# Kernel tuning notes

Hardware: AMD Instinct MI355X
Metric: run time of the kernel (lower is better)

The kernel has to match this reference:

```python
import jax, jax.numpy as jnp
import numpy as np

STATE_DIM, ACTION_DIM, HIDDEN_DIM = 512, 64, 2048
INPUT_DIM = STATE_DIM + ACTION_DIM + 1  # 577
BATCH = 4096


def setup_inputs() -> dict:
    key = jax.random.key(0)
    ks = jax.random.split(key, 12)
    sc_x = 1.0 / np.sqrt(INPUT_DIM)
    sc_h = 1.0 / np.sqrt(HIDDEN_DIM)
    return {
        "s": jax.random.normal(ks[0], (BATCH, STATE_DIM), jnp.float32),
        "a_prev": jax.random.normal(ks[1], (BATCH, ACTION_DIM), jnp.float32),
        "r_prev": jax.random.normal(ks[2], (BATCH, 1), jnp.float32),
        "h": jnp.zeros((HIDDEN_DIM,), jnp.float32),
        "c": jnp.zeros((HIDDEN_DIM,), jnp.float32),
        # Fused gate weights: columns ordered [i, f, g(c-tilde), o]
        "Wx": jax.random.uniform(ks[3], (INPUT_DIM, 4 * HIDDEN_DIM), jnp.float32, -sc_x, sc_x),
        "Wh": jax.random.uniform(ks[4], (HIDDEN_DIM, 4 * HIDDEN_DIM), jnp.float32, -sc_h, sc_h),
        "bh": jax.random.uniform(ks[5], (4 * HIDDEN_DIM,), jnp.float32, -sc_h, sc_h),
        "Wa": jax.random.uniform(ks[6], (HIDDEN_DIM, ACTION_DIM), jnp.float32, -sc_h, sc_h),
        "ba": jax.random.uniform(ks[7], (ACTION_DIM,), jnp.float32, -sc_h, sc_h),
        "Wv": jax.random.uniform(ks[8], (HIDDEN_DIM, 1), jnp.float32, -sc_h, sc_h),
        "bv": jax.random.uniform(ks[9], (1,), jnp.float32, -sc_h, sc_h),
    }


def reference(s, a_prev, r_prev, h, c, Wx, Wh, bh, Wa, ba, Wv, bv):
    # x: [B, input_dim]
    x = jnp.concatenate([s, a_prev, r_prev], axis=1)
    # Two fused GEMMs replace the 8 separate small linears (same math).
    z = x @ Wx + h @ Wh + bh          # [B, 4H]
    zi, zf, zg, zo = jnp.split(z, 4, axis=-1)
    i = jax.nn.sigmoid(zi)
    f = jax.nn.sigmoid(zf)
    c_new = f * c + i * jnp.tanh(zg)  # [B, H] (c broadcast over batch)
    o = jax.nn.sigmoid(zo)
    h_new = o * jnp.tanh(c_new)       # [B, H]
    probs = jax.nn.softmax(h_new @ Wa + ba, axis=1)  # [B, A]
    v = h_new @ Wv + bv               # [B, 1]
    return (probs, v)
```

## Files before the change

kernel.cpp:

```cpp
#include <hip/hip_runtime.h>
#include <hip/hip_bf16.h>

#define BATCH   4096
#define SDIM    512
#define ADIM    64
#define IDIM    577
#define KP2     640
#define NKT2    10
#define HDIM    2048
#define ZDIM    8192
#define BUFE    (128 * 64)

typedef __attribute__((ext_vector_type(8))) __bf16 bf16x8;
typedef __attribute__((ext_vector_type(4))) float  accx4;

__global__ __launch_bounds__(256) void setup_kernel(
    const float* __restrict__ s, const float* __restrict__ a_prev,
    const float* __restrict__ r_prev, const float* __restrict__ h,
    const float* __restrict__ wx, const float* __restrict__ wh,
    const float* __restrict__ wa,
    __hip_bfloat16* __restrict__ xb, __hip_bfloat16* __restrict__ wxt,
    __hip_bfloat16* __restrict__ waT, float* __restrict__ zh_w)
{
    __shared__ float stile[64 * 33];
    const int bid = blockIdx.x;
    const int t = threadIdx.x;

    if (bid < 2560) {
        const int kt2 = bid >> 8;
        const int nt  = bid & 255;
        const int c  = t & 31, r0 = t >> 5;
#pragma unroll
        for (int i = 0; i < 8; ++i) {
            int r = r0 + i * 8;
            int k = kt2 * 64 + r;
            stile[r * 33 + c] =
                (k < IDIM) ? wx[(size_t)k * ZDIM + nt * 32 + c] : 0.0f;
        }
        __syncthreads();
        const int nr = t >> 3, ch = t & 7;
        bf16x8 w8;
#pragma unroll
        for (int j = 0; j < 8; ++j)
            w8[j] = (__bf16)stile[(ch * 8 + j) * 33 + nr];
        *(bf16x8*)(wxt + (size_t)(nt * 32 + nr) * KP2 + kt2 * 64 + ch * 8) = w8;
    } else if (bid < 2816) {
        const int zb = bid - 2560;
        const int nb = zb & 31, ky = zb >> 5;
        const int n  = nb * 256 + t;
        const float* hp  = h + ky * 256;
        const float* whp = wh + (size_t)ky * 256 * ZDIM + n;
        float p = 0.0f;
#pragma unroll 16
        for (int kk = 0; kk < 256; ++kk)
            p = fmaf(hp[kk], whp[(size_t)kk * ZDIM], p);
        zh_w[ky * ZDIM + n] = p;
    } else if (bid < 6912) {
        const int row = bid - 2816;
        const float* srow = s + (size_t)row * SDIM;
        const float* arow = a_prev + (size_t)row * ADIM;
        __hip_bfloat16* xrow = xb + (size_t)row * KP2;
        for (int c = t; c < KP2; c += 256) {
            float v;
            if (c < SDIM)        v = srow[c];
            else if (c < 576)    v = arow[c - SDIM];
            else if (c == 576)   v = r_prev[row];
            else                 v = 0.0f;
            xrow[c] = __float2bfloat16(v);
        }
    } else {
        const int wb = bid - 6912;
        const int kt = wb >> 1, at = wb & 1;
        const int c  = t & 31, r0 = t >> 5;
#pragma unroll
        for (int i = 0; i < 4; ++i) {
            int r = r0 + i * 8;
            stile[r * 33 + c] = wa[(size_t)(kt * 32 + r) * ADIM + at * 32 + c];
        }
        __syncthreads();
#pragma unroll
        for (int i = 0; i < 4; ++i) {
            int r = r0 + i * 8;
            waT[(size_t)(at * 32 + r) * HDIM + kt * 32 + c] =
                __float2bfloat16(stile[c * 33 + r]);
        }
    }
}

__device__ __forceinline__ float sigmoid_f(float x) {
    return 1.0f / (1.0f + __expf(-x));
}
__device__ __forceinline__ float tanh_f(float x) {
    return 1.0f - 2.0f / (1.0f + __expf(2.0f * x));
}

__global__ __launch_bounds__(256, 2) void lstm_gemm(
    const __hip_bfloat16* __restrict__ xb,
    const __hip_bfloat16* __restrict__ wxt,
    const float* __restrict__ zh_w,
    const float* __restrict__ bh,
    const float* __restrict__ cvec,
    __hip_bfloat16* __restrict__ hout)
{
    __shared__ __bf16 smA[2 * BUFE];
    __shared__ __bf16 smB[2 * BUFE];
    const int t    = threadIdx.x;
    const int lane = t & 63;
    const int wid  = t >> 6;
    const int m0   = blockIdx.x * 128;
    const int n0   = blockIdx.y * 32;
    const int wm   = wid >> 1, wn = wid & 1;
    const int fl15 = lane & 15;
    const int fhi  = lane >> 4;

    accx4 acc[4][4] = {};

    const int srow = lane >> 3;
    const int slot = lane & 7;
    const int cch  = slot ^ srow;
    const __bf16* gA[4]; const __bf16* gB[4];
    __bf16* lA[4]; __bf16* lB[4];
#pragma unroll
    for (int i = 0; i < 4; ++i) {
        const int r = wid * 32 + i * 8 + srow;
        gA[i] = (const __bf16*)xb + (size_t)(m0 + r) * KP2 + cch * 8;
        const int g = r >> 5, nn = r & 31;
        gB[i] = (const __bf16*)wxt +
                (size_t)(g * HDIM + n0 + nn) * KP2 + cch * 8;
        lA[i] = smA + (wid * 32 + i * 8) * 64;
        lB[i] = smB + (wid * 32 + i * 8) * 64;
    }

    auto stage = [&](int tile, int p) {
        const int ko = tile * 64;
        const int po = p * BUFE;
#pragma unroll
        for (int i = 0; i < 4; ++i) {
            __builtin_amdgcn_global_load_lds(
                (const __attribute__((address_space(1))) void*)(gA[i] + ko),
                (__attribute__((address_space(3))) void*)(lA[i] + po),
                16, 0, 0);
            __builtin_amdgcn_global_load_lds(
                (const __attribute__((address_space(1))) void*)(gB[i] + ko),
                (__attribute__((address_space(3))) void*)(lB[i] + po),
                16, 0, 0);
        }
    };

    auto compute = [&](int p) {
        const int po = p * BUFE;
#pragma unroll
        for (int hf = 0; hf < 2; ++hf) {
            const int sl = ((hf * 4 + fhi) ^ slot) * 8;
            bf16x8 af[4], bfr[4];
#pragma unroll
            for (int rt = 0; rt < 4; ++rt)
                af[rt] = *(const bf16x8*)(smA + po +
                    (wm * 64 + rt * 16 + fl15) * 64 + sl);
#pragma unroll
            for (int g = 0; g < 4; ++g)
                bfr[g] = *(const bf16x8*)(smB + po +
                    (g * 32 + wn * 16 + fl15) * 64 + sl);
#pragma unroll
            for (int g = 0; g < 4; ++g)
#pragma unroll
                for (int rt = 0; rt < 4; ++rt)
                    acc[g][rt] = __builtin_amdgcn_mfma_f32_16x16x32_bf16(
                        af[rt], bfr[g], acc[g][rt], 0, 0, 0);
        }
    };

    stage(0, 0);
    __syncthreads();
#pragma unroll
    for (int kt = 0; kt < NKT2 - 1; ++kt) {
        stage(kt + 1, (kt + 1) & 1);
        compute(kt & 1);
        __syncthreads();
    }
    compute((NKT2 - 1) & 1);

    const int colg = n0 + wn * 16 + fl15;
    float zsum[4];
#pragma unroll
    for (int g = 0; g < 4; ++g) {
        float z = bh[g * HDIM + colg];
#pragma unroll
        for (int j = 0; j < 8; ++j)
            z += zh_w[j * ZDIM + g * HDIM + colg];
        zsum[g] = z;
    }
    const float cv = cvec[colg];
#pragma unroll
    for (int rt = 0; rt < 4; ++rt) {
#pragma unroll
        for (int r = 0; r < 4; ++r) {
            const int row = m0 + wm * 64 + rt * 16 + (fhi << 2) + r;
            const float zi = acc[0][rt][r] + zsum[0];
            const float zf = acc[1][rt][r] + zsum[1];
            const float zg = acc[2][rt][r] + zsum[2];
            const float zo = acc[3][rt][r] + zsum[3];
            const float cn = sigmoid_f(zf) * cv + sigmoid_f(zi) * tanh_f(zg);
            const float hn = sigmoid_f(zo) * tanh_f(cn);
            hout[(size_t)row * HDIM + colg] = __float2bfloat16(hn);
        }
    }
}

__global__ __launch_bounds__(512) void head_kernel(
    const __hip_bfloat16* __restrict__ hnew,
    const __hip_bfloat16* __restrict__ waT,
    const float* __restrict__ wv,
    const float* __restrict__ ba, const float* __restrict__ bv,
    float* __restrict__ probs, float* __restrict__ vout)
{
    __shared__ float lg[2][16][68];
    __shared__ float vpart[2][16];
    const int t    = threadIdx.x;
    const int lane = t & 63;
    const int wid  = t >> 6;
    const int kh   = wid >> 2;
    const int wid2 = wid & 3;
    const int r0   = blockIdx.x * 16;
    const int fl15 = lane & 15, fhi = lane >> 4;

    const __bf16* arow = (const __bf16*)hnew +
        (size_t)(r0 + fl15) * HDIM + kh * 1024 + fhi * 8;
    const __bf16* brow = (const __bf16*)waT +
        (size_t)(wid2 * 16 + fl15) * HDIM + kh * 1024 + fhi * 8;
    const float* wvp = wv + kh * 1024 + fhi * 8;
    const bool do_v = (wid2 == 0);

    accx4 acc0 = {}, acc1 = {};
    float vacc = 0.0f;
#pragma unroll 4
    for (int kk = 0; kk < 1024; kk += 64) {
        bf16x8 a0 = *(const bf16x8*)(arow + kk);
        bf16x8 b0 = *(const bf16x8*)(brow + kk);
        bf16x8 a1 = *(const bf16x8*)(arow + kk + 32);
        bf16x8 b1 = *(const bf16x8*)(brow + kk + 32);
        acc0 = __builtin_amdgcn_mfma_f32_16x16x32_bf16(a0, b0, acc0, 0, 0, 0);
        acc1 = __builtin_amdgcn_mfma_f32_16x16x32_bf16(a1, b1, acc1, 0, 0, 0);
        if (do_v) {
#pragma unroll
            for (int j = 0; j < 8; ++j) {
                vacc = fmaf((float)a0[j], wvp[kk + j], vacc);
                vacc = fmaf((float)a1[j], wvp[kk + 32 + j], vacc);
            }
        }
    }
#pragma unroll
    for (int r = 0; r < 4; ++r)
        lg[kh][fhi * 4 + r][wid2 * 16 + fl15] = acc0[r] + acc1[r];
    if (do_v) {
        vacc += __shfl_xor(vacc, 16);
        vacc += __shfl_xor(vacc, 32);
        if (lane < 16) vpart[kh][lane] = vacc;
    }
    __syncthreads();

    const float bav = ba[lane];
#pragma unroll
    for (int i = 0; i < 2; ++i) {
        const int row = wid * 2 + i;
        const float logit = lg[0][row][lane] + lg[1][row][lane] + bav;
        float m = logit;
#pragma unroll
        for (int mask = 32; mask >= 1; mask >>= 1)
            m = fmaxf(m, __shfl_xor(m, mask));
        const float e = __expf(logit - m);
        float ssum = e;
#pragma unroll
        for (int mask = 32; mask >= 1; mask >>= 1)
            ssum += __shfl_xor(ssum, mask);
        probs[(size_t)(r0 + row) * 64 + lane] = e / ssum;
    }
    if (t < 16) vout[r0 + t] = vpart[0][t] + vpart[1][t] + bv[0];
}

extern "C" void kernel_launch(void* const* d_in, const int* in_sizes, int n_in,
                              void* d_out, int out_size, void* d_ws,
                              size_t ws_size, hipStream_t stream)
{
    const float* s      = (const float*)d_in[0];
    const float* a_prev = (const float*)d_in[1];
    const float* r_prev = (const float*)d_in[2];
    const float* h      = (const float*)d_in[3];
    const float* c      = (const float*)d_in[4];
    const float* Wx     = (const float*)d_in[5];
    const float* Wh     = (const float*)d_in[6];
    const float* bh     = (const float*)d_in[7];
    const float* Wa     = (const float*)d_in[8];
    const float* ba     = (const float*)d_in[9];
    const float* Wv     = (const float*)d_in[10];
    const float* bv     = (const float*)d_in[11];

    float* out   = (float*)d_out;
    float* probs = out;
    float* vout  = out + (size_t)BATCH * ADIM;

    char* ws = (char*)d_ws;
    __hip_bfloat16* xb   = (__hip_bfloat16*)ws;
    __hip_bfloat16* wxt  = (__hip_bfloat16*)(ws + 5242880);
    __hip_bfloat16* waT  = (__hip_bfloat16*)(ws + 15728640);
    float* zh_w          = (float*)(ws + 15990784);
    __hip_bfloat16* hnew = (__hip_bfloat16*)(ws + 16252928);

    setup_kernel<<<7040, 256, 0, stream>>>(
        s, a_prev, r_prev, h, Wx, Wh, Wa, xb, wxt, waT, zh_w);
    lstm_gemm<<<dim3(BATCH / 128, HDIM / 32), 256, 0, stream>>>(
        xb, wxt, zh_w, bh, c, hnew);
    head_kernel<<<BATCH / 16, 512, 0, stream>>>(
        hnew, waT, Wv, ba, bv, probs, vout);
}
```

Baseline: 231.7 us.

## Halve GEMM K-tile, raise occupancy, widen Wx transpose, pre-reduce zh

```diff
diff --git a/kernel.cpp b/kernel.cpp
--- a/kernel.cpp
+++ b/kernel.cpp
@@ -6,10 +6,10 @@
 #define ADIM    64
 #define IDIM    577
 #define KP2     640
-#define NKT2    10
+#define NKT     20
 #define HDIM    2048
 #define ZDIM    8192
-#define BUFE    (128 * 64)
+#define BUFE    (128 * 32)
 
 typedef __attribute__((ext_vector_type(8))) __bf16 bf16x8;
 typedef __attribute__((ext_vector_type(4))) float  accx4;
@@ -22,30 +22,38 @@
     __hip_bfloat16* __restrict__ xb, __hip_bfloat16* __restrict__ wxt,
     __hip_bfloat16* __restrict__ waT, float* __restrict__ zh_w)
 {
-    __shared__ float stile[64 * 33];
+    __shared__ float stile[64 * 65];
     const int bid = blockIdx.x;
     const int t = threadIdx.x;
 
-    if (bid < 2560) {
-        const int kt2 = bid >> 8;
-        const int nt  = bid & 255;
-        const int c  = t & 31, r0 = t >> 5;
-#pragma unroll
-        for (int i = 0; i < 8; ++i) {
-            int r = r0 + i * 8;
-            int k = kt2 * 64 + r;
-            stile[r * 33 + c] =
-                (k < IDIM) ? wx[(size_t)k * ZDIM + nt * 32 + c] : 0.0f;
+    if (bid < 1280) {
+        const int kt2 = bid >> 7;
+        const int nt  = bid & 127;
+        const int c4  = t & 15;
+        const int rr  = t >> 4;
+#pragma unroll
+        for (int i = 0; i < 4; ++i) {
+            const int r = rr + i * 16;
+            const int k = kt2 * 64 + r;
+            float4 v = (k < IDIM)
+                ? *(const float4*)(wx + (size_t)k * ZDIM + nt * 64 + c4 * 4)
+                : float4{0.f, 0.f, 0.f, 0.f};
+            *(float4*)(stile + r * 65 + c4 * 4) = v;
         }
         __syncthreads();
-        const int nr = t >> 3, ch = t & 7;
-        bf16x8 w8;
-#pragma unroll
-        for (int j = 0; j < 8; ++j)
-            w8[j] = (__bf16)stile[(ch * 8 + j) * 33 + nr];
-        *(bf16x8*)(wxt + (size_t)(nt * 32 + nr) * KP2 + kt2 * 64 + ch * 8) = w8;
-    } else if (bid < 2816) {
-        const int zb = bid - 2560;
+        const int ch = t & 7;
+#pragma unroll
+        for (int i = 0; i < 2; ++i) {
+            const int nr = (t >> 3) + i * 32;
+            bf16x8 w8;
+#pragma unroll
+            for (int j = 0; j < 8; ++j)
+                w8[j] = (__bf16)stile[(ch * 8 + j) * 65 + nr];
+            *(bf16x8*)(wxt + (size_t)(nt * 64 + nr) * KP2 + kt2 * 64 + ch * 8)
+                = w8;
+        }
+    } else if (bid < 1536) {
+        const int zb = bid - 1280;
         const int nb = zb & 31, ky = zb >> 5;
         const int n  = nb * 256 + t;
         const float* hp  = h + ky * 256;
@@ -55,8 +63,8 @@
         for (int kk = 0; kk < 256; ++kk)
             p = fmaf(hp[kk], whp[(size_t)kk * ZDIM], p);
         zh_w[ky * ZDIM + n] = p;
-    } else if (bid < 6912) {
-        const int row = bid - 2816;
+    } else if (bid < 5632) {
+        const int row = bid - 1536;
         const float* srow = s + (size_t)row * SDIM;
         const float* arow = a_prev + (size_t)row * ADIM;
         __hip_bfloat16* xrow = xb + (size_t)row * KP2;
@@ -69,7 +77,7 @@
             xrow[c] = __float2bfloat16(v);
         }
     } else {
-        const int wb = bid - 6912;
+        const int wb = bid - 5632;
         const int kt = wb >> 1, at = wb & 1;
         const int c  = t & 31, r0 = t >> 5;
 #pragma unroll
@@ -87,6 +95,18 @@
     }
 }
 
+__global__ __launch_bounds__(256) void zh_reduce(
+    const float* __restrict__ zh_w, const float* __restrict__ bh,
+    float* __restrict__ zh)
+{
+    const int j = blockIdx.x * 256 + threadIdx.x;
+    float v = bh[j];
+#pragma unroll
+    for (int p = 0; p < 8; ++p)
+        v += zh_w[p * ZDIM + j];
+    zh[j] = v;
+}
+
 __device__ __forceinline__ float sigmoid_f(float x) {
     return 1.0f / (1.0f + __expf(-x));
 }
@@ -94,11 +114,10 @@
     return 1.0f - 2.0f / (1.0f + __expf(2.0f * x));
 }
 
-__global__ __launch_bounds__(256, 2) void lstm_gemm(
+__global__ __launch_bounds__(256, 3) void lstm_gemm(
     const __hip_bfloat16* __restrict__ xb,
     const __hip_bfloat16* __restrict__ wxt,
-    const float* __restrict__ zh_w,
-    const float* __restrict__ bh,
+    const float* __restrict__ zh,
     const float* __restrict__ cvec,
     __hip_bfloat16* __restrict__ hout)
 {
@@ -115,91 +134,81 @@
 
     accx4 acc[4][4] = {};
 
-    const int srow = lane >> 3;
-    const int slot = lane & 7;
-    const int cch  = slot ^ srow;
-    const __bf16* gA[4]; const __bf16* gB[4];
-    __bf16* lA[4]; __bf16* lB[4];
-#pragma unroll
-    for (int i = 0; i < 4; ++i) {
-        const int r = wid * 32 + i * 8 + srow;
+    const int cch = (lane & 3) ^ ((lane >> 2) & 3) ^ ((lane >> 4) & 3);
+    const __bf16* gA[2]; const __bf16* gB[2]; int lofs[2];
+#pragma unroll
+    for (int i = 0; i < 2; ++i) {
+        const int rbase = wid * 32 + i * 16;
+        const int r = rbase + (lane >> 2);
         gA[i] = (const __bf16*)xb + (size_t)(m0 + r) * KP2 + cch * 8;
         const int g = r >> 5, nn = r & 31;
         gB[i] = (const __bf16*)wxt +
                 (size_t)(g * HDIM + n0 + nn) * KP2 + cch * 8;
-        lA[i] = smA + (wid * 32 + i * 8) * 64;
-        lB[i] = smB + (wid * 32 + i * 8) * 64;
+        lofs[i] = rbase * 32;
     }
 
     auto stage = [&](int tile, int p) {
-        const int ko = tile * 64;
+        const int ko = tile * 32;
         const int po = p * BUFE;
 #pragma unroll
-        for (int i = 0; i < 4; ++i) {
+        for (int i = 0; i < 2; ++i) {
             __builtin_amdgcn_global_load_lds(
                 (const __attribute__((address_space(1))) void*)(gA[i] + ko),
-                (__attribute__((address_space(3))) void*)(lA[i] + po),
+                (__attribute__((address_space(3))) void*)(smA + po + lofs[i]),
                 16, 0, 0);
             __builtin_amdgcn_global_load_lds(
                 (const __attribute__((address_space(1))) void*)(gB[i] + ko),
-                (__attribute__((address_space(3))) void*)(lB[i] + po),
+                (__attribute__((address_space(3))) void*)(smB + po + lofs[i]),
                 16, 0, 0);
         }
     };
+
+    const int sl = ((fhi ^ (fl15 & 3) ^ ((fl15 >> 2) & 3)) * 8);
 
     auto compute = [&](int p) {
         const int po = p * BUFE;
-#pragma unroll
-        for (int hf = 0; hf < 2; ++hf) {
-            const int sl = ((hf * 4 + fhi) ^ slot) * 8;
-            bf16x8 af[4], bfr[4];
+        bf16x8 af[4], bfr[4];
+#pragma unroll
+        for (int rt = 0; rt < 4; ++rt)
+            af[rt] = *(const bf16x8*)(smA + po +
+                (wm * 64 + rt * 16 + fl15) * 32 + sl);
+#pragma unroll
+        for (int g = 0; g < 4; ++g)
+            bfr[g] = *(const bf16x8*)(smB + po +
+                (g * 32 + wn * 16 + fl15) * 32 + sl);
+#pragma unroll
+        for (int g = 0; g < 4; ++g)
 #pragma unroll
             for (int rt = 0; rt < 4; ++rt)
-                af[rt] = *(const bf16x8*)(smA + po +
-                    (wm * 64 + rt * 16 + fl15) * 64 + sl);
-#pragma unroll
-            for (int g = 0; g < 4; ++g)
-                bfr[g] = *(const bf16x8*)(smB + po +
-                    (g * 32 + wn * 16 + fl15) * 64 + sl);
-#pragma unroll
-            for (int g = 0; g < 4; ++g)
-#pragma unroll
-                for (int rt = 0; rt < 4; ++rt)
-                    acc[g][rt] = __builtin_amdgcn_mfma_f32_16x16x32_bf16(
-                        af[rt], bfr[g], acc[g][rt], 0, 0, 0);
-        }
+                acc[g][rt] = __builtin_amdgcn_mfma_f32_16x16x32_bf16(
+                    af[rt], bfr[g], acc[g][rt], 0, 0, 0);
     };
 
     stage(0, 0);
     __syncthreads();
 #pragma unroll
-    for (int kt = 0; kt < NKT2 - 1; ++kt) {
+    for (int kt = 0; kt < NKT - 1; ++kt) {
         stage(kt + 1, (kt + 1) & 1);
         compute(kt & 1);
         __syncthreads();
     }
-    compute((NKT2 - 1) & 1);
+    compute((NKT - 1) & 1);
 
     const int colg = n0 + wn * 16 + fl15;
-    float zsum[4];
-#pragma unroll
-    for (int g = 0; g < 4; ++g) {
-        float z = bh[g * HDIM + colg];
-#pragma unroll
-        for (int j = 0; j < 8; ++j)
-            z += zh_w[j * ZDIM + g * HDIM + colg];
-        zsum[g] = z;
-    }
-    const float cv = cvec[colg];
+    const float zhi = zh[colg];
+    const float zhf = zh[HDIM + colg];
+    const float zhg = zh[2 * HDIM + colg];
+    const float zho = zh[3 * HDIM + colg];
+    const float cv  = cvec[colg];
 #pragma unroll
     for (int rt = 0; rt < 4; ++rt) {
 #pragma unroll
         for (int r = 0; r < 4; ++r) {
             const int row = m0 + wm * 64 + rt * 16 + (fhi << 2) + r;
-            const float zi = acc[0][rt][r] + zsum[0];
-            const float zf = acc[1][rt][r] + zsum[1];
-            const float zg = acc[2][rt][r] + zsum[2];
-            const float zo = acc[3][rt][r] + zsum[3];
+            const float zi = acc[0][rt][r] + zhi;
+            const float zf = acc[1][rt][r] + zhf;
+            const float zg = acc[2][rt][r] + zhg;
+            const float zo = acc[3][rt][r] + zho;
             const float cn = sigmoid_f(zf) * cv + sigmoid_f(zi) * tanh_f(zg);
             const float hn = sigmoid_f(zo) * tanh_f(cn);
             hout[(size_t)row * HDIM + colg] = __float2bfloat16(hn);
@@ -232,7 +241,7 @@
     const bool do_v = (wid2 == 0);
 
     accx4 acc0 = {}, acc1 = {};
-    float vacc = 0.0f;
+    float va0 = 0.f, va1 = 0.f, va2 = 0.f, va3 = 0.f;
 #pragma unroll 4
     for (int kk = 0; kk < 1024; kk += 64) {
         bf16x8 a0 = *(const bf16x8*)(arow + kk);
@@ -243,9 +252,15 @@
         acc1 = __builtin_amdgcn_mfma_f32_16x16x32_bf16(a1, b1, acc1, 0, 0, 0);
         if (do_v) {
 #pragma unroll
-            for (int j = 0; j < 8; ++j) {
-                vacc = fmaf((float)a0[j], wvp[kk + j], vacc);
-                vacc = fmaf((float)a1[j], wvp[kk + 32 + j], vacc);
+            for (int j = 0; j < 8; j += 4) {
+                va0 = fmaf((float)a0[j],     wvp[kk + j],          va0);
+                va1 = fmaf((float)a0[j + 1], wvp[kk + j + 1],      va1);
+                va2 = fmaf((float)a0[j + 2], wvp[kk + j + 2],      va2);
+                va3 = fmaf((float)a0[j + 3], wvp[kk + j + 3],      va3);
+                va0 = fmaf((float)a1[j],     wvp[kk + 32 + j],     va0);
+                va1 = fmaf((float)a1[j + 1], wvp[kk + 32 + j + 1], va1);
+                va2 = fmaf((float)a1[j + 2], wvp[kk + 32 + j + 2], va2);
+                va3 = fmaf((float)a1[j + 3], wvp[kk + 32 + j + 3], va3);
             }
         }
     }
@@ -253,6 +268,7 @@
     for (int r = 0; r < 4; ++r)
         lg[kh][fhi * 4 + r][wid2 * 16 + fl15] = acc0[r] + acc1[r];
     if (do_v) {
+        float vacc = (va0 + va1) + (va2 + va3);
         vacc += __shfl_xor(vacc, 16);
         vacc += __shfl_xor(vacc, 32);
         if (lane < 16) vpart[kh][lane] = vacc;
@@ -304,12 +320,14 @@
     __hip_bfloat16* wxt  = (__hip_bfloat16*)(ws + 5242880);
     __hip_bfloat16* waT  = (__hip_bfloat16*)(ws + 15728640);
     float* zh_w          = (float*)(ws + 15990784);
-    __hip_bfloat16* hnew = (__hip_bfloat16*)(ws + 16252928);
-
-    setup_kernel<<<7040, 256, 0, stream>>>(
+    float* zh            = (float*)(ws + 16252928);
+    __hip_bfloat16* hnew = (__hip_bfloat16*)(ws + 16285696);
+
+    setup_kernel<<<5760, 256, 0, stream>>>(
         s, a_prev, r_prev, h, Wx, Wh, Wa, xb, wxt, waT, zh_w);
+    zh_reduce<<<ZDIM / 256, 256, 0, stream>>>(zh_w, bh, zh);
     lstm_gemm<<<dim3(BATCH / 128, HDIM / 32), 256, 0, stream>>>(
-        xb, wxt, zh_w, bh, c, hnew);
+        xb, wxt, zh, c, hnew);
     head_kernel<<<BATCH / 16, 512, 0, stream>>>(
         hnew, waT, Wv, ba, bv, probs, vout);
 }
```

Measured after the change: 220.7 us. 1.05x faster.
